# Kernel optimization log

Measured on AMD Instinct MI355X. Metric: run time of the kernel, lower is better.

Reference implementation:

```python
import jax, jax.numpy as jnp
import numpy as np

DIM = 512
HID = 2048
BLOCKS = 4
VOCAB = 32000
HEADS = 8
HD = DIM // HEADS
B = 4
T = 257
MBS = 64
LR = 3e-4
EPS = 1e-5


def setup_inputs() -> dict:
    key = jax.random.key(0)
    ks = jax.random.split(key, 10)
    s = 0.02
    n = lambda k, shp: jax.random.normal(k, shp, dtype=jnp.float32) * s
    return {
        'x': jax.random.randint(ks[0], (B, T), 0, VOCAB),
        'embed': n(ks[1], (VOCAB, DIM)),
        'pos': n(ks[2], (MBS, DIM)),
        'ln1_g': jnp.ones((BLOCKS, DIM), jnp.float32),
        'ln1_b': jnp.zeros((BLOCKS, DIM), jnp.float32),
        'qkv_w': n(ks[3], (BLOCKS, DIM, 3 * DIM)),
        'qkv_b': jnp.zeros((BLOCKS, 3 * DIM), jnp.float32),
        'proj_w': n(ks[4], (BLOCKS, DIM, DIM)),
        'proj_b': jnp.zeros((BLOCKS, DIM), jnp.float32),
        'ln2_g': jnp.ones((BLOCKS, DIM), jnp.float32),
        'ln2_b': jnp.zeros((BLOCKS, DIM), jnp.float32),
        'mlp_w1': n(ks[5], (BLOCKS, DIM, HID)),
        'mlp_b1': jnp.zeros((BLOCKS, HID), jnp.float32),
        'mlp_w2': n(ks[6], (BLOCKS, HID, DIM)),
        'mlp_b2': jnp.zeros((BLOCKS, DIM), jnp.float32),
        'lnf_g': jnp.ones((DIM,), jnp.float32),
        'lnf_b': jnp.zeros((DIM,), jnp.float32),
        'head_w': n(ks[7], (DIM, VOCAB)),
        'head_b': jnp.zeros((VOCAB,), jnp.float32),
    }


def _ln(x, g, b):
    m = x.mean(-1, keepdims=True)
    v = ((x - m) ** 2).mean(-1, keepdims=True)
    return (x - m) * jax.lax.rsqrt(v + EPS) * g + b


def _transformer(tokens, static, dyn):
    (embed, pos, ln1_g, ln1_b, qkv_w, qkv_b, proj_w, proj_b,
     ln2_g, ln2_b, lnf_g, lnf_b, head_w, head_b) = static
    mw1, mb1, mw2, mb2 = dyn
    Bx, L = tokens.shape
    h = embed[tokens] + pos[:L]                      # [B, L, D]
    mask = jnp.tril(jnp.ones((L, L), dtype=bool))
    for i in range(BLOCKS):
        xn = _ln(h, ln1_g[i], ln1_b[i])
        qkv = xn @ qkv_w[i] + qkv_b[i]               # [B, L, 3D]
        q, k, v = jnp.split(qkv, 3, axis=-1)
        hd = lambda t: t.reshape(Bx, L, HEADS, HD).transpose(0, 2, 1, 3)
        q, k, v = hd(q), hd(k), hd(v)                # [B, H, L, Dh]
        s = jnp.einsum('bhqd,bhkd->bhqk', q, k) / np.float32(np.sqrt(HD))
        s = jnp.where(mask, s, jnp.float32(-1e9))
        a = jax.nn.softmax(s, axis=-1)
        o = jnp.einsum('bhqk,bhkd->bhqd', a, v).transpose(0, 2, 1, 3).reshape(Bx, L, DIM)
        h = h + o @ proj_w[i] + proj_b[i]
        xn2 = _ln(h, ln2_g[i], ln2_b[i])
        h = h + jax.nn.gelu(xn2 @ mw1[i] + mb1[i]) @ mw2[i] + mb2[i]
    h = _ln(h, lnf_g, lnf_b)
    return h @ head_w + head_b                       # [B, L, V]


def reference(x, embed, pos, ln1_g, ln1_b, qkv_w, qkv_b, proj_w, proj_b,
              ln2_g, ln2_b, mlp_w1, mlp_b1, mlp_w2, mlp_b2,
              lnf_g, lnf_b, head_w, head_b):
    static = (embed, pos, ln1_g, ln1_b, qkv_w, qkv_b, proj_w, proj_b,
              ln2_g, ln2_b, lnf_g, lnf_b, head_w, head_b)
    dyn0 = (mlp_w1, mlp_b1, mlp_w2, mlp_b2)
    n_chunks = (T - 1) // MBS
    inp = x[:, :T - 1].reshape(B, n_chunks, MBS).transpose(1, 0, 2)  # [C, B, b]
    tgt = x[:, 1:T].reshape(B, n_chunks, MBS).transpose(1, 0, 2)

    def step(dyn, chunk):
        ci, ct = chunk
        def loss_fn(d):
            logits = _transformer(ci, static, d)
            logp = jax.nn.log_softmax(logits, axis=-1)
            nll = -jnp.take_along_axis(logp, ct[..., None], axis=-1).squeeze(-1).mean()
            return nll, logits
        grads, logits = jax.grad(loss_fn, has_aux=True)(dyn)
        new_dyn = jax.tree_util.tree_map(lambda p, g: p - LR * g, dyn, grads)
        return new_dyn, logits

    _, logit_chunks = jax.lax.scan(step, dyn0, (inp, tgt))   # [C, B, b, V]
    return logit_chunks.transpose(1, 0, 2, 3).reshape(B, (T - 1), VOCAB)
```

## Files before the change

### kernel.cpp

```cpp
#include <hip/hip_runtime.h>
#include <cstddef>

#define LRATE 3e-4f

typedef short short8 __attribute__((ext_vector_type(8)));
typedef float f32x4 __attribute__((ext_vector_type(4)));
typedef __bf16 bf16x8 __attribute__((ext_vector_type(8)));

__device__ __forceinline__ unsigned short f2b(float f){
  unsigned u = __builtin_bit_cast(unsigned, f);
  unsigned r = (u + 0x7fffu + ((u>>16)&1u)) >> 16;
  return (unsigned short)r;
}
__device__ __forceinline__ float b2f(unsigned short s){
  unsigned u = ((unsigned)s)<<16;
  return __builtin_bit_cast(float, u);
}
__device__ __forceinline__ float gelu_f(float x){
  float u = 0.7978845608028654f*(x + 0.044715f*x*x*x);
  float t = tanhf(u);
  return 0.5f*x*(1.f+t);
}
__device__ __forceinline__ float gelu_df(float x){
  float x2 = x*x;
// ... 89 lines not shown

  STAGE(0,0);
  for(int t=0;t<k_iters;++t){
    int buf=t&1;
    STAGE(t+1<k_iters?t+1:t, buf^1);
    asm volatile("" ::: "memory");
    constexpr int VMC = LNA ? (TILE/32) : (TILE/16);
    if constexpr(VMC==2)      asm volatile("s_waitcnt vmcnt(2)" ::: "memory");
    else if constexpr(VMC==4) asm volatile("s_waitcnt vmcnt(4)" ::: "memory");
    else                      asm volatile("s_waitcnt vmcnt(8)" ::: "memory");
    __builtin_amdgcn_sched_barrier(0);
    __builtin_amdgcn_s_barrier();
    asm volatile("" ::: "memory");
    const char* Ab=(const char*)(Asm+buf*TILE*64);
    const char* Bb=(const char*)(Bsm+buf*TILE*64);
    #pragma unroll
    for(int h=0;h<2;h++){
      bf16x8 af[F], bfr[F];
      #pragma unroll
      for(int fa=0;fa<F;fa++){
        int row=wr*(TILE/2)+fa*16+r16;
        int c=(h*4+kg)^(row&7);
        af[fa]=__builtin_bit_cast(bf16x8, *(const short8*)(Ab + row*128 + c*16));
      }
      #pragma unroll
      for(int fb=0;fb<F;fb++){
        int row=wc*(TILE/2)+fb*16+r16;
        int c=(h*4+kg)^(row&7);
        bfr[fb]=__builtin_bit_cast(bf16x8, *(const short8*)(Bb + row*128 + c*16));
      }
      #pragma unroll
      for(int fa=0;fa<F;fa++)
        #pragma unroll
        for(int fb=0;fb<F;fb++)
          acc[fa][fb]=__builtin_amdgcn_mfma_f32_16x16x32_bf16(af[fa],bfr[fb],acc[fa][fb],0,0,0);
    }
    asm volatile("s_waitcnt lgkmcnt(0)" ::: "memory");
    __builtin_amdgcn_sched_barrier(0);
    __builtin_amdgcn_s_barrier();
    asm volatile("" ::: "memory");
  }
  asm volatile("s_waitcnt vmcnt(0)" ::: "memory");

  int rb = lane>>4;
  float st1[F][4]={}, st2[F][4]={};
  #pragma unroll
  for(int fa=0; fa<F; fa++){
    #pragma unroll
    for(int fb=0; fb<F; fb++){
      f32x4 av = acc[fa][fb];
      #pragma unroll
      for(int i=0;i<4;i++){
        int m = bm + wr*(TILE/2) + fa*16 + rb*4 + i;
        int n = bn + wc*(TILE/2) + fb*16 + r16;
        float v = av[i];
        if(bias) v += bias[n];
        if(resid) v += resid[(size_t)m*N + n];
        if(zsrc) v *= gelu_df(zsrc[(size_t)m*N + n]);
        if constexpr(STATS){ st1[fa][i] += v; st2[fa][i] += v*v; }
        int mo = (remap_c>=0)? ((m>>6)*256 + remap_c*64 + (m&63)) : m;
        if(outf) outf[(size_t)blockIdx.z*M*N + (size_t)mo*N + n] = v;
        if(outb) outb[(size_t)mo*N + n] = f2b(gelu_b ? gelu_f(v) : v);
      }
    }
  }
  if constexpr(STATS){
    #pragma unroll
    for(int fa=0; fa<F; fa++){
      #pragma unroll
      for(int i=0;i<4;i++){
        float s1 = st1[fa][i], s2 = st2[fa][i];
        #pragma unroll
        for(int msk=1; msk<16; msk<<=1){ s1 += __shfl_xor(s1,msk); s2 += __shfl_xor(s2,msk); }
        if(r16==0){
          int m = bm + wr*(TILE/2) + fa*16 + rb*4 + i;
          atomicAdd(&oS1[m], s1);
          atomicAdd(&oS2[m], s2);
        }
      }
    }
  }
}

template<int LNA, int STATS>
__global__ __launch_bounds__(256) void k_nt32(
    const unsigned short* __restrict__ Ag,
    const float* __restrict__ Af, const float* __restrict__ aS1, const float* __restrict__ aS2,
    const float* __restrict__ lng, const float* __restrict__ lnb,
    const unsigned short* __restrict__ Bg,
    const float* __restrict__ bias, const float* __restrict__ resid, const float* __restrict__ zsrc,
    float* __restrict__ outf, unsigned short* __restrict__ outb,
    float* __restrict__ oS1, float* __restrict__ oS2,
    int M, int N, int K, int k_iters, int gelu_b)
{
  __shared__ __align__(16) short Asl[8*2048];
  __shared__ __align__(16) short Bsl[8*2048];
  int tid=threadIdx.x, lane=tid&63, w=tid>>6;
  int wr=w>>1, wc=w&1, r16=lane&15, kg=lane>>4;
  int bn=blockIdx.x*32, bm=blockIdx.y*32;
  int row=tid>>3, s8=tid&7, gc=s8^(row&7);
  f32x4 acc={0.f,0.f,0.f,0.f};

  auto ISSUE_A=[&](int t,int slot){
    gll16(Ag + (size_t)(bm+row)*K + t*64 + gc*8, (char*)Asl + slot*4096 + tid*16);
  };
  auto ISSUE_B=[&](int t,int slot){
    gll16(Bg + (size_t)(bn+row)*K + t*64 + gc*8, (char*)Bsl + slot*4096 + tid*16);
  };

  if constexpr(LNA){
    float mm, rr;
    { float a=aS1[bm+row], b=aS2[bm+row]; mm=a*(1.f/512.f); rr=rsqrtf(b*(1.f/512.f)-mm*mm+1e-5f); }
    for(int t=0;t<k_iters;t++){
      const float* src = Af + (size_t)(bm+row)*K + t*64 + gc*8;
      float4 v0=*(const float4*)src, v1=*(const float4*)(src+4);
      const float* gp=lng+t*64+gc*8; const float* bp=lnb+t*64+gc*8;
      float4 g0=*(const float4*)gp, g1=*(const float4*)(gp+4);
      float4 c0=*(const float4*)bp, c1=*(const float4*)(bp+4);
      short8 o;
      o[0]=(short)f2b((v0.x-mm)*rr*g0.x+c0.x);
      o[1]=(short)f2b((v0.y-mm)*rr*g0.y+c0.y);
      o[2]=(short)f2b((v0.z-mm)*rr*g0.z+c0.z);
      o[3]=(short)f2b((v0.w-mm)*rr*g0.w+c0.w);
      o[4]=(short)f2b((v1.x-mm)*rr*g1.x+c1.x);
      o[5]=(short)f2b((v1.y-mm)*rr*g1.y+c1.y);
      o[6]=(short)f2b((v1.z-mm)*rr*g1.z+c1.z);
      o[7]=(short)f2b((v1.w-mm)*rr*g1.w+c1.w);
      *(short8*)((char*)Asl + t*4096 + tid*16) = o;
    }
  }

  #pragma unroll
  for(int s=0;s<6;s++){
    if constexpr(LNA==0) ISSUE_A(s, s);
    ISSUE_B(s, s);
  }
  if constexpr(LNA){
    asm volatile("s_waitcnt lgkmcnt(0)" ::: "memory");
    __builtin_amdgcn_sched_barrier(0);
    __builtin_amdgcn_s_barrier();
  }

  for(int t=0;t<k_iters;++t){
    int tt = (t+6<k_iters)? t+6 : k_iters-1;
    int slot=(t+6)&7;
    if constexpr(LNA==0) ISSUE_A(tt, slot);
    ISSUE_B(tt, slot);
    if constexpr(LNA==0) asm volatile("s_waitcnt vmcnt(12)" ::: "memory");
    else                 asm volatile("s_waitcnt vmcnt(6)" ::: "memory");
    __builtin_amdgcn_sched_barrier(0);
    __builtin_amdgcn_s_barrier();
    __builtin_amdgcn_sched_barrier(0);
    const char* Ab = LNA ? (const char*)Asl + t*4096 : (const char*)Asl + (t&7)*4096;
    const char* Bb = (const char*)Bsl + (t&7)*4096;
    #pragma unroll
    for(int h=0;h<2;h++){
      int rowa=wr*16+r16, ca=(h*4+kg)^(rowa&7);
      bf16x8 a=__builtin_bit_cast(bf16x8, *(const short8*)(Ab + rowa*128 + ca*16));
      int rowb=wc*16+r16, cb=(h*4+kg)^(rowb&7);
      bf16x8 b=__builtin_bit_cast(bf16x8, *(const short8*)(Bb + rowb*128 + cb*16));
      acc=__builtin_amdgcn_mfma_f32_16x16x32_bf16(a,b,acc,0,0,0);
    }
    asm volatile("s_waitcnt lgkmcnt(0)" ::: "memory");
    __builtin_amdgcn_sched_barrier(0);
  }
  asm volatile("s_waitcnt vmcnt(0)" ::: "memory");

  int rb=lane>>4;
  float st1[4]={}, st2[4]={};
  #pragma unroll
  for(int i=0;i<4;i++){
    int m = bm + wr*16 + rb*4 + i;
    int n = bn + wc*16 + r16;
    float v = acc[i];
    if(bias) v += bias[n];
    if(resid) v += resid[(size_t)m*N + n];
    if(zsrc) v *= gelu_df(zsrc[(size_t)m*N + n]);
    if constexpr(STATS){ st1[i]=v; st2[i]=v*v; }
    if(outf) outf[(size_t)m*N + n] = v;
    if(outb) outb[(size_t)m*N + n] = f2b(gelu_b ? gelu_f(v) : v);
  }
  if constexpr(STATS){
    #pragma unroll
    for(int i=0;i<4;i++){
      float s1=st1[i], s2=st2[i];
      #pragma unroll
      for(int msk=1;msk<16;msk<<=1){ s1+=__shfl_xor(s1,msk); s2+=__shfl_xor(s2,msk); }
      if(r16==0){
        int m = bm + wr*16 + rb*4 + i;
        atomicAdd(&oS1[m], s1);
        atomicAdd(&oS2[m], s2);
      }
    }
  }
}

template<int LNA>
__device__ __forceinline__ void sgd_body(
    const unsigned short* __restrict__ Ag,
    const float* __restrict__ Af, const float* __restrict__ aS1, const float* __restrict__ aS2,
    const float* __restrict__ lng, const float* __restrict__ lnb,
    const unsigned short* __restrict__ Bg,
    float* __restrict__ Wf, unsigned short* __restrict__ Wb, unsigned short* __restrict__ Wt,
    float* __restrict__ bv, int M, int N, int bm, int bn,
    short* Asm, short* Bsm, short* Tsm)
{
  int tid = threadIdx.x;
  f32x4 acc00={},acc01={},acc10={},acc11={};
  int lane = tid&63, w = tid>>6, wr = w>>1, wc = w&1;
  int r16 = lane&15, kg = lane>>4;
  float gv[8], bvv[8];
  if constexpr(LNA){
    int ms=(tid&7)*8;
    #pragma unroll
    for(int j=0;j<8;j++){ gv[j]=lng[bm+ms+j]; bvv[j]=lnb[bm+ms+j]; }
  }
  float csum = 0.f;
  int docs = (bv && bm==0 && tid<64);
  for(int k0=0; k0<256; k0+=32){
    if constexpr(LNA==0){
      int kk = tid>>3, ms=(tid&7)*8;
      short8 v = *(const short8*)(Ag + (size_t)(k0+kk)*M + bm + ms);
      #pragma unroll
      for(int j=0;j<8;j++){ int row=ms+j; Asm[row*40 + (((kk>>3)^((row>>3)&3))<<3) + (kk&7)] = v[j]; }
    } else {
      int kk = tid>>3, ms=(tid&7)*8;
      int token = k0+kk;
      float s1=aS1[token], s2=aS2[token];
      float mm=s1*(1.f/512.f);
      float rr=rsqrtf(s2*(1.f/512.f)-mm*mm+1e-5f);
      const float* src = Af + (size_t)token*M + bm + ms;
      float4 v0=*(const float4*)src, v1=*(const float4*)(src+4);
      float vals[8]={v0.x,v0.y,v0.z,v0.w,v1.x,v1.y,v1.z,v1.w};
      #pragma unroll
      for(int j=0;j<8;j++){
        int row=ms+j;
// ... 253 lines not shown
    __builtin_amdgcn_sched_barrier(0);
  }
  asm volatile("s_waitcnt vmcnt(0)" ::: "memory");
  __syncthreads();

  #pragma unroll
  for(int fa=0;fa<2;fa++)
    #pragma unroll
    for(int fb=0;fb<3;fb++)
      #pragma unroll
      for(int i=0;i<4;i++){
        int row=wr*32+fa*16+rb*4+i;
        int band=wc*3+fb;
        int p=band>>2, cin=(band&3)*16+r16;
        float v = acc[fa][fb][i] + bias[p*512 + hh*64 + cin];
        unsigned short bv16 = f2b(v);
        qkB[(size_t)(bb*64+row)*1536 + p*512 + hh*64 + cin] = bv16;
        if(p==0)      tr_write(Qs,  row, cin, bv16);
        else if(p==1) tr_write(Ks2, row, cin, bv16);
        else          tr_write(Vt,  cin, row, bv16);
      }
  __syncthreads();

  int wr2=w>>2, wc2=w&3;
  f32x4 sa[2]={};
  #pragma unroll
  for(int h=0;h<2;h++){
    bf16x8 bfr = frag_read(Ks2, wc2*16+r16, h, kg);
    #pragma unroll
    for(int fa=0;fa<2;fa++){
      bf16x8 af = frag_read(Qs, wr2*32+fa*16+r16, h, kg);
      sa[fa]=__builtin_amdgcn_mfma_f32_16x16x32_bf16(af,bfr,sa[fa],0,0,0);
    }
  }
  #pragma unroll
  for(int fa=0;fa<2;fa++)
    #pragma unroll
    for(int i=0;i<4;i++){
      int row=wr2*32+fa*16+rb*4+i, col=wc2*16+r16;
      Sf[row*68+col] = (col<=row) ? sa[fa][i]*0.125f : -1e9f;
    }
  __syncthreads();

  {
    int srow=tid>>3, seg8=tid&7;
    float vals[8]; float mx=-3.4e38f;
    #pragma unroll
    for(int k2=0;k2<8;k2++){ vals[k2]=Sf[srow*68+seg8*8+k2]; mx=fmaxf(mx,vals[k2]); }
    mx=fmaxf(mx,__shfl_xor(mx,1)); mx=fmaxf(mx,__shfl_xor(mx,2)); mx=fmaxf(mx,__shfl_xor(mx,4));
    float sm=0;
    #pragma unroll
    for(int k2=0;k2<8;k2++){ vals[k2]=expf(vals[k2]-mx); sm+=vals[k2]; }
    sm+=__shfl_xor(sm,1); sm+=__shfl_xor(sm,2); sm+=__shfl_xor(sm,4);
    float inv=1.f/sm;
    short8 p0;
    #pragma unroll
    for(int k2=0;k2<8;k2++) p0[k2]=(short)f2b(vals[k2]*inv);
    __syncthreads();
    *(short8*)((char*)Pb + srow*128 + (((seg8)^(srow&7))<<4)) = p0;
    *(short8*)(ap + ((size_t)(bb*8+hh)*64 + srow)*64 + seg8*8) = p0;
  }
  __syncthreads();

  f32x4 oa[2]={};
  #pragma unroll
  for(int h=0;h<2;h++){
    bf16x8 bfr = frag_read(Vt, wc2*16+r16, h, kg);
    #pragma unroll
    for(int fa=0;fa<2;fa++){
      bf16x8 af = frag_read(Pb, wr2*32+fa*16+r16, h, kg);
      oa[fa]=__builtin_amdgcn_mfma_f32_16x16x32_bf16(af,bfr,oa[fa],0,0,0);
    }
  }
  #pragma unroll
  for(int fa=0;fa<2;fa++)
    #pragma unroll
    for(int i=0;i<4;i++){
      int row=wr2*32+fa*16+rb*4+i, col=wc2*16+r16;
      obuf[(size_t)(bb*64+row)*512 + hh*64 + col] = f2b(oa[fa][i]);
    }
}

__global__ __launch_bounds__(512) void k_do_attn(
    const unsigned short* __restrict__ dhBb, const unsigned short* __restrict__ projwB,
    const unsigned short* __restrict__ qkvB, const unsigned short* __restrict__ ap,
    unsigned short* __restrict__ dqkv)
{
  __shared__ __align__(16) short Asl[4*4096];
  __shared__ __align__(16) short Bsl2[4*4096];
  __shared__ __align__(16) short dOs[4096], Vs[4096], Kt[4096], Qt[4096], dOt[4096], Pt[4096], dsN[4096], dsT[4096];
  __shared__ float rsum[64][2];
  float* Pacc = (float*)Asl;
  int hh=blockIdx.x, bb=blockIdx.y;
  int tid=threadIdx.x, lane=tid&63, w=tid>>6;
  int wg=w>>2, wl=w&3;
  int wr=wl>>1, wc=wl&1, r16=lane&15, kg=lane>>4, rb=lane>>4;
  const unsigned short* qbase = qkvB + (size_t)bb*64*1536 + hh*64;
  const unsigned short* abase = ap + (size_t)(bb*8+hh)*64*64;

  {
    int row=tid>>3, gc=(tid&7)^(row&7);
    gll16(qbase + 1024 + (size_t)row*1536 + gc*8, (char*)Vs + tid*16);
  }
  {
    int row=tid>>3, c8=tid&7;
    short8 kreg=*(const short8*)(qbase+512+(size_t)row*1536+c8*8);
    short8 qreg=*(const short8*)(qbase+(size_t)row*1536+c8*8);
    short8 preg=*(const short8*)(abase+(size_t)row*64+c8*8);
    #pragma unroll
    for(int j=0;j<8;j++){
      int col=c8*8+j;
      tr_write(Kt, col, row, (unsigned short)kreg[j]);
      tr_write(Qt, col, row, (unsigned short)qreg[j]);
      tr_write(Pt, col, row, (unsigned short)preg[j]);
    }
  }

  const unsigned short* Bg = projwB + (size_t)(hh*64)*512;
  auto STAGE=[&](int t,int buf){
    int k0=(wg*4+t)*64;
    #pragma unroll
    for(int q=0;q<2;q++){
      int id=wl*128+q*64+lane, row=id>>3, gc=(id&7)^(row&7);
      gll16(dhBb + (size_t)(bb*64+row)*512 + k0 + gc*8, (char*)Asl + (wg*2+buf)*8192 + id*16);
      gll16(Bg + (size_t)row*512 + k0 + gc*8, (char*)Bsl2 + (wg*2+buf)*8192 + id*16);
    }
  };
  STAGE(0,0);
  f32x4 acc[2][2]={};
  for(int t=0;t<4;t++){
    int buf=t&1;
    STAGE(t+1<4?t+1:t, buf^1);
    asm volatile("s_waitcnt vmcnt(4)" ::: "memory");
    __builtin_amdgcn_sched_barrier(0);
    __builtin_amdgcn_s_barrier();
    __builtin_amdgcn_sched_barrier(0);
    const char* Ab=(const char*)Asl + (wg*2+buf)*8192;
    const char* Bb=(const char*)Bsl2 + (wg*2+buf)*8192;
    #pragma unroll
    for(int h=0;h<2;h++){
      bf16x8 af[2], bfr[2];
      #pragma unroll
      for(int f=0;f<2;f++){
        int rowa=wr*32+f*16+r16, ca=(h*4+kg)^(rowa&7);
        af[f]=__builtin_bit_cast(bf16x8, *(const short8*)(Ab + rowa*128 + ca*16));
        int rowb=wc*32+f*16+r16, cb=(h*4+kg)^(rowb&7);
        bfr[f]=__builtin_bit_cast(bf16x8, *(const short8*)(Bb + rowb*128 + cb*16));
      }
      #pragma unroll
      for(int fa=0;fa<2;fa++)
        #pragma unroll
        for(int fb=0;fb<2;fb++)
          acc[fa][fb]=__builtin_amdgcn_mfma_f32_16x16x32_bf16(af[fa],bfr[fb],acc[fa][fb],0,0,0);
    }
    asm volatile("s_waitcnt lgkmcnt(0)" ::: "memory");
    __builtin_amdgcn_sched_barrier(0);
    __builtin_amdgcn_s_barrier();
    __builtin_amdgcn_sched_barrier(0);
  }
  asm volatile("s_waitcnt vmcnt(0)" ::: "memory");
  __syncthreads();

  if(wg==1){
    #pragma unroll
    for(int fa=0;fa<2;fa++)
      #pragma unroll
      for(int fb=0;fb<2;fb++)
        #pragma unroll
        for(int i=0;i<4;i++){
          int row=wr*32+fa*16+rb*4+i, col=wc*32+fb*16+r16;
          Pacc[row*64+col]=acc[fa][fb][i];
        }
  }
  __syncthreads();
  if(wg==0){
    #pragma unroll
    for(int fa=0;fa<2;fa++)
      #pragma unroll
      for(int fb=0;fb<2;fb++)
        #pragma unroll
        for(int i=0;i<4;i++){
          int row=wr*32+fa*16+rb*4+i, col=wc*32+fb*16+r16;
          unsigned short db = f2b(acc[fa][fb][i] + Pacc[row*64+col]);
          tr_write(dOs, row, col, db);
          tr_write(dOt, col, row, db);
        }
  }
  __syncthreads();

  f32x4 da[2][2]={};
  float pv[2][2][4];
  if(wg==0){
    #pragma unroll
    for(int h=0;h<2;h++){
      bf16x8 af[2], bfr[2];
      #pragma unroll
      for(int f=0;f<2;f++){ af[f]=frag_read(dOs, wr*32+f*16+r16, h, kg); bfr[f]=frag_read(Vs, wc*32+f*16+r16, h, kg); }
      #pragma unroll
      for(int fa=0;fa<2;fa++)
        #pragma unroll
        for(int fb=0;fb<2;fb++)
          da[fa][fb]=__builtin_amdgcn_mfma_f32_16x16x32_bf16(af[fa],bfr[fb],da[fa][fb],0,0,0);
    }
    float part[2][4]={};
    #pragma unroll
    for(int fa=0;fa<2;fa++)
      #pragma unroll
      for(int i=0;i<4;i++){
        #pragma unroll
        for(int fb=0;fb<2;fb++){
          int row=wr*32+fa*16+rb*4+i, col=wc*32+fb*16+r16;
          float p = b2f(*(const unsigned short*)((const char*)Pt + col*128 + (((row>>3)^(col&7))<<4) + (row&7)*2));
          pv[fa][fb][i]=p;
          part[fa][i] += p*da[fa][fb][i];
        }
        float s=part[fa][i];
        #pragma unroll
        for(int msk=1;msk<16;msk<<=1) s += __shfl_xor(s,msk);
        if(r16==0) rsum[wr*32+fa*16+rb*4+i][wc]=s;
      }
  } else {
    f32x4 dvv[2][2]={};
    #pragma unroll
    for(int h=0;h<2;h++){
      bf16x8 af[2], bfr[2];
      #pragma unroll
      for(int f=0;f<2;f++){ af[f]=frag_read(Pt, wr*32+f*16+r16, h, kg); bfr[f]=frag_read(dOt, wc*32+f*16+r16, h, kg); }
      #pragma unroll
      for(int fa=0;fa<2;fa++)
        #pragma unroll
        for(int fb=0;fb<2;fb++)
          dvv[fa][fb]=__builtin_amdgcn_mfma_f32_16x16x32_bf16(af[fa],bfr[fb],dvv[fa][fb],0,0,0);
    }
    #pragma unroll
    for(int fa=0;fa<2;fa++)
      #pragma unroll
      for(int fb=0;fb<2;fb++)
        #pragma unroll
        for(int i=0;i<4;i++){
          int row=wr*32+fa*16+rb*4+i, col=wc*32+fb*16+r16;
          dqkv[(size_t)(bb*64+row)*1536 + hh*64 + 1024 + col] = f2b(dvv[fa][fb][i]);
        }
  }
  __syncthreads();

  if(wg==0){
    #pragma unroll
    for(int fa=0;fa<2;fa++)
      #pragma unroll
      for(int fb=0;fb<2;fb++)
        #pragma unroll
        for(int i=0;i<4;i++){
          int row=wr*32+fa*16+rb*4+i, col=wc*32+fb*16+r16;
          float rt = rsum[row][0]+rsum[row][1];
          float ds = pv[fa][fb][i]*(da[fa][fb][i]-rt)*0.125f;
// ... 49 lines not shown
  #pragma unroll
  for(int off=32;off;off>>=1) mx = fmaxf(mx, __shfl_xor(mx,off));
  if(lane==0) red[w]=mx;
  __syncthreads();
  float m = red[0];
  #pragma unroll
  for(int i=1;i<16;i++) m = fmaxf(m, red[i]);
  __syncthreads();

  float s=0;
  for(int v=tid; v<32000; v+=1024){ float e = expf(b2f(eb[v])-m); s+=e; eb[v]=f2b(e); }
  #pragma unroll
  for(int off=32;off;off>>=1) s += __shfl_xor(s,off);
  if(lane==0) red[w]=s;
  __syncthreads();
  float tot = 0.f;
  #pragma unroll
  for(int i=0;i<16;i++) tot += red[i];
  float iz = 1.f/tot * (1.f/256.f);

  unsigned short* dr = dlog + (size_t)n*32000;
  for(int v=tid; v<32000; v+=1024){
    float a = b2f(eb[v])*iz;
    if(v==tgt) a -= (1.f/256.f);
    dr[v] = f2b(a);
  }
}

extern "C" void kernel_launch(void* const* d_in, const int* in_sizes, int n_in,
                              void* d_out, int out_size, void* d_ws, size_t ws_size,
                              hipStream_t stream)
{
  const int*   x      = (const int*)d_in[0];
  const float* embed  = (const float*)d_in[1];
  const float* pos    = (const float*)d_in[2];
  const float* ln1_g  = (const float*)d_in[3];
  const float* ln1_b  = (const float*)d_in[4];
  const float* qkv_w  = (const float*)d_in[5];
  const float* qkv_b  = (const float*)d_in[6];
  const float* proj_w = (const float*)d_in[7];
  const float* proj_b = (const float*)d_in[8];
  const float* ln2_g  = (const float*)d_in[9];
  const float* ln2_b  = (const float*)d_in[10];
  const float* mlp_w1 = (const float*)d_in[11];
  const float* mlp_b1 = (const float*)d_in[12];
  const float* mlp_w2 = (const float*)d_in[13];
  const float* mlp_b2 = (const float*)d_in[14];
  const float* lnf_g  = (const float*)d_in[15];
  const float* lnf_b  = (const float*)d_in[16];
  const float* head_w = (const float*)d_in[17];
  const float* head_b = (const float*)d_in[18];
  float* out = (float*)d_out;

  char* base = (char*)d_ws;
  size_t off = 0;
  auto AB = [&](size_t bytes)->char*{ char* p = base + off; off += (bytes + 255) & ~(size_t)255; return p; };
  float* W1c  = (float*)AB(16777216);
  float* W2c  = (float*)AB(16777216);
  float* B1c  = (float*)AB(32768);
  float* B2c  = (float*)AB(8192);
  float* hin  = (float*)AB(5*524288);
  float* h1s  = (float*)AB(4*524288);
  float* z1s  = (float*)AB(4*2097152);
  float* dhA  = (float*)AB(524288);
  float* dhB  = (float*)AB(524288);
  float* dxn  = (float*)AB(524288);
  float* dpart= (float*)AB(50*524288);
  float* stats= (float*)AB(4*9*2*256*4);
  unsigned short* qkvwB = (unsigned short*)AB(6291456);
  unsigned short* qkvwT = (unsigned short*)AB(6291456);
  unsigned short* projwB= (unsigned short*)AB(2097152);
  unsigned short* projwT= (unsigned short*)AB(2097152);
  unsigned short* headwB= (unsigned short*)AB(32768000);
  unsigned short* headwT= (unsigned short*)AB(32768000);
  unsigned short* W1b   = (unsigned short*)AB(8388608);
  unsigned short* W1t   = (unsigned short*)AB(8388608);
  unsigned short* W2b   = (unsigned short*)AB(8388608);
  unsigned short* W2t   = (unsigned short*)AB(8388608);
  unsigned short* z1gs  = (unsigned short*)AB(4194304);
  unsigned short* qkBs  = (unsigned short*)AB(4*786432);
  unsigned short* apBs  = (unsigned short*)AB(4*262144);
  unsigned short* obufB = (unsigned short*)AB(262144);
  unsigned short* dlogB = (unsigned short*)AB(16384000);
  unsigned short* dhbB  = (unsigned short*)AB(5*262144);
  unsigned short* dhBb  = (unsigned short*)AB(262144);
  unsigned short* dz1bs = (unsigned short*)AB(4*1048576);
  unsigned short* dqkvB = (unsigned short*)AB(786432);

  auto SS1 = [&](int c, int s)->float*{ return stats + ((size_t)(c*9+s)*2)*256; };
  auto SS2 = [&](int c, int s)->float*{ return stats + ((size_t)(c*9+s)*2)*256 + 256; };

  k_setup<<<72,256,0,stream>>>(stats, B1c, mlp_b1, B2c, mlp_b2);
  k_cvt_t<<<dim3(24,8,4),256,0,stream>>>(qkv_w, qkvwT, qkvwB, nullptr, 512, 1536);
  k_cvt_t<<<dim3(8,8,4),256,0,stream>>>(proj_w, projwT, projwB, nullptr, 512, 512);
  k_cvt_t<<<dim3(500,8,1),256,0,stream>>>(head_w, headwT, headwB, nullptr, 512, 32000);
  k_cvt_t<<<dim3(32,8,4),256,0,stream>>>(mlp_w1, W1t, W1b, W1c, 512, 2048);
  k_cvt_t<<<dim3(8,32,4),256,0,stream>>>(mlp_w2, W2t, W2b, W2c, 2048, 512);

  for(int c=0;c<4;c++){
    k_embed<<<256,256,0,stream>>>(x, embed, pos, hin, SS1(c,0), SS2(c,0), c);
    for(int i=0;i<4;i++){
      float* h0 = hin + (size_t)i*131072;
      float* h2 = hin + (size_t)(i+1)*131072;
      float* h1 = h1s + (size_t)i*131072;
      float* z1 = z1s + (size_t)i*524288;
      unsigned short* z1g = z1gs + (size_t)i*524288;
      unsigned short* qkB = qkBs + (size_t)i*393216;
      unsigned short* apB = apBs + (size_t)i*131072;
      k_qkv_attn<<<dim3(8,4),512,0,stream>>>(h0, SS1(c,i), SS2(c,i), ln1_g+i*512, ln1_b+i*512,
          qkvwT+(size_t)i*786432, qkv_b+i*1536, qkB, obufB, apB);
      k_nt32<0,1><<<dim3(16,8),256,0,stream>>>(obufB, nullptr, nullptr, nullptr, nullptr, nullptr,
          projwT+(size_t)i*262144, proj_b+i*512, h0, nullptr,
          h1, nullptr, SS1(c,5+i), SS2(c,5+i), 256,512,512, 8, 0);
      k_nt32<1,0><<<dim3(64,8),256,0,stream>>>(nullptr, h1, SS1(c,5+i), SS2(c,5+i), ln2_g+i*512, ln2_b+i*512,
          W1t+(size_t)i*1048576, B1c+i*2048, nullptr, nullptr,
          z1, z1g, nullptr, nullptr, 256,2048,512, 8, 1);
      k_nt32<0,1><<<dim3(16,8),256,0,stream>>>(z1g, nullptr, nullptr, nullptr, nullptr, nullptr,
          W2t+(size_t)i*1048576, B2c+i*512, h1, nullptr,
          h2, nullptr, SS1(c,i+1), SS2(c,i+1), 256,512,2048, 32, 0);
    }
    k_nt<128,1,0><<<dim3(250,2),256,0,stream>>>(nullptr, hin+4*131072, SS1(c,4), SS2(c,4), lnf_g, lnf_b,
        headwT, head_b, nullptr, nullptr,
        out, nullptr, nullptr, nullptr, 256,32000,512, 8, 0, c);

    k_ce_dlog<<<256,1024,0,stream>>>(out, x, dlogB, c);
    k_nt<128,0,0><<<dim3(4,2,50),256,0,stream>>>(dlogB, nullptr, nullptr, nullptr, nullptr, nullptr,
        headwB, nullptr, nullptr, nullptr,
        dpart, nullptr, nullptr, nullptr, 256,512,32000, 10, 0, -1);
    k_ln_bwd<<<256,256,0,stream>>>(nullptr, dpart, 50, hin+4*131072, lnf_g, SS1(c,4), SS2(c,4),
        nullptr, dhA, dhbB + 3*131072);
    for(int i=3;i>=0;i--){
      float* h0 = hin + (size_t)i*131072;
      float* h1 = h1s + (size_t)i*131072;
      float* z1 = z1s + (size_t)i*524288;
      unsigned short* qkB = qkBs + (size_t)i*393216;
      unsigned short* apB = apBs + (size_t)i*131072;
      k_nt32<0,0><<<dim3(64,8),256,0,stream>>>(dhbB + (size_t)i*131072, nullptr, nullptr, nullptr, nullptr, nullptr,
          W2b+(size_t)i*1048576, nullptr, nullptr, z1,
          nullptr, dz1bs + (size_t)i*524288, nullptr, nullptr, 256,2048,512, 8, 0);
      k_nt32<0,0><<<dim3(16,8),256,0,stream>>>(dz1bs + (size_t)i*524288, nullptr, nullptr, nullptr, nullptr, nullptr,
          W1b+(size_t)i*1048576, nullptr, nullptr, nullptr,
          dxn, nullptr, nullptr, nullptr, 256,512,2048, 32, 0);
      k_ln_bwd<<<256,256,0,stream>>>(dxn, nullptr, 0, h1, ln2_g+i*512, SS1(c,5+i), SS2(c,5+i),
          dhA, dhB, dhBb);
      k_do_attn<<<dim3(8,4),512,0,stream>>>(dhBb, projwB+(size_t)i*262144, qkB, apB, dqkvB);
      k_nt32<0,0><<<dim3(16,8),256,0,stream>>>(dqkvB, nullptr, nullptr, nullptr, nullptr, nullptr,
          qkvwB+(size_t)i*786432, nullptr, nullptr, nullptr,
          dxn, nullptr, nullptr, nullptr, 256,512,1536, 24, 0);
      k_ln_bwd<<<256,256,0,stream>>>(dxn, nullptr, 0, h0, ln1_g+i*512, SS1(c,i), SS2(c,i),
          dhB, dhA, dhbB + (size_t)((i==0)?4:i-1)*131072);
    }
    k_sgd_all<<<2048,256,0,stream>>>(z1gs, dhbB, dz1bs, h1s, stats, c,
        W1c, W1b, W1t, B1c, W2c, W2b, W2t, B2c, ln2_g, ln2_b);
  }
}
```

Baseline: 2.364 ms.

## Fuse LayerNorm backward into the following backward GEMM and attention kernels

Removes the standalone k_ln_bwd launches in the backward pass. LN2 backward is computed inside k_do_attn's prologue, which builds the bf16 A operand in shared memory. LN1 backward of the next-higher layer moves into a new LNB variant of k_nt32 that builds its bf16 A tile in LDS. One block per row tile also writes the fp32 and bf16 residual gradients to global memory. This trades fewer launches and intermediate round trips for redundant LN-backward recomputation in every column block, plus higher LDS use in k_do_attn.

```diff
diff --git a/kernel.cpp b/kernel.cpp
--- a/kernel.cpp
+++ b/kernel.cpp
@@ -195,7 +195,7 @@
   }
 }
 
-template<int LNA, int STATS>
+template<int LNA, int STATS, int LNB>
 __global__ __launch_bounds__(256) void k_nt32(
     const unsigned short* __restrict__ Ag,
     const float* __restrict__ Af, const float* __restrict__ aS1, const float* __restrict__ aS2,
@@ -204,6 +204,8 @@
     const float* __restrict__ bias, const float* __restrict__ resid, const float* __restrict__ zsrc,
     float* __restrict__ outf, unsigned short* __restrict__ outb,
     float* __restrict__ oS1, float* __restrict__ oS2,
+    const float* __restrict__ dyf, const float* __restrict__ adn,
+    float* __restrict__ oA, unsigned short* __restrict__ oB2,
     int M, int N, int K, int k_iters, int gelu_b)
 {
   __shared__ __align__(16) short Asl[8*2048];
@@ -220,6 +222,62 @@
   auto ISSUE_B=[&](int t,int slot){
     gll16(Bg + (size_t)(bn+row)*K + t*64 + gc*8, (char*)Bsl + slot*4096 + tid*16);
   };
+
+  if constexpr(LNB){
+    #pragma unroll
+    for(int s=0;s<6;s++) ISSUE_B(s, s);
+    int grow = bm + row;
+    float s1v=aS1[grow], s2v=aS2[grow];
+    float m=s1v*(1.f/512.f);
+    float r=rsqrtf(s2v*(1.f/512.f)-m*m+1e-5f);
+    float sgh=0.f, sghx=0.f;
+    for(int t=0;t<k_iters;t++){
+      const float* dyp=dyf+(size_t)grow*512+t*64+gc*8;
+      const float* xp =Af +(size_t)grow*512+t*64+gc*8;
+      const float* gp =lng+t*64+gc*8;
+      float4 a0=*(const float4*)dyp, a1=*(const float4*)(dyp+4);
+      float4 x0=*(const float4*)xp,  x1=*(const float4*)(xp+4);
+      float4 g0=*(const float4*)gp,  g1=*(const float4*)(gp+4);
+      float dys[8]={a0.x,a0.y,a0.z,a0.w,a1.x,a1.y,a1.z,a1.w};
+      float xs[8]={x0.x,x0.y,x0.z,x0.w,x1.x,x1.y,x1.z,x1.w};
+      float gs[8]={g0.x,g0.y,g0.z,g0.w,g1.x,g1.y,g1.z,g1.w};
+      #pragma unroll
+      for(int j=0;j<8;j++){ float gh=dys[j]*gs[j]; float xh=(xs[j]-m)*r; sgh+=gh; sghx+=gh*xh; }
+    }
+    sgh +=__shfl_xor(sgh,1);  sgh +=__shfl_xor(sgh,2);  sgh +=__shfl_xor(sgh,4);
+    sghx+=__shfl_xor(sghx,1); sghx+=__shfl_xor(sghx,2); sghx+=__shfl_xor(sghx,4);
+    float mg=sgh*(1.f/512.f), mgx=sghx*(1.f/512.f);
+    for(int t=0;t<k_iters;t++){
+      const float* dyp=dyf+(size_t)grow*512+t*64+gc*8;
+      const float* xp =Af +(size_t)grow*512+t*64+gc*8;
+      const float* gp =lng+t*64+gc*8;
+      const float* ap2=adn+(size_t)grow*512+t*64+gc*8;
+      float4 a0=*(const float4*)dyp, a1=*(const float4*)(dyp+4);
+      float4 x0=*(const float4*)xp,  x1=*(const float4*)(xp+4);
+      float4 g0=*(const float4*)gp,  g1=*(const float4*)(gp+4);
+      float4 d0=*(const float4*)ap2, d1=*(const float4*)(ap2+4);
+      float dys[8]={a0.x,a0.y,a0.z,a0.w,a1.x,a1.y,a1.z,a1.w};
+      float xs[8]={x0.x,x0.y,x0.z,x0.w,x1.x,x1.y,x1.z,x1.w};
+      float gs[8]={g0.x,g0.y,g0.z,g0.w,g1.x,g1.y,g1.z,g1.w};
+      float ads[8]={d0.x,d0.y,d0.z,d0.w,d1.x,d1.y,d1.z,d1.w};
+      float dv[8];
+      short8 o;
+      #pragma unroll
+      for(int j=0;j<8;j++){
+        float gh=dys[j]*gs[j]; float xh=(xs[j]-m)*r;
+        dv[j]=(gh-mg-xh*mgx)*r + ads[j];
+        o[j]=(short)f2b(dv[j]);
+      }
+      *(short8*)((char*)Asl + t*4096 + tid*16) = o;
+      if(blockIdx.x==0){
+        float4 w0={dv[0],dv[1],dv[2],dv[3]}, w1={dv[4],dv[5],dv[6],dv[7]};
+        *(float4*)(oA+(size_t)grow*512+t*64+gc*8) = w0;
+        *(float4*)(oA+(size_t)grow*512+t*64+gc*8+4) = w1;
+        *(short8*)(oB2+(size_t)grow*512+t*64+gc*8) = o;
+      }
+    }
+    __syncthreads();
+  }
 
   if constexpr(LNA){
     float mm, rr;
@@ -243,10 +301,12 @@
     }
   }
 
-  #pragma unroll
-  for(int s=0;s<6;s++){
-    if constexpr(LNA==0) ISSUE_A(s, s);
-    ISSUE_B(s, s);
+  if constexpr(!LNB){
+    #pragma unroll
+    for(int s=0;s<6;s++){
+      if constexpr(LNA==0) ISSUE_A(s, s);
+      ISSUE_B(s, s);
+    }
   }
   if constexpr(LNA){
     asm volatile("s_waitcnt lgkmcnt(0)" ::: "memory");
@@ -254,17 +314,18 @@
     __builtin_amdgcn_s_barrier();
   }
 
+  constexpr int ARES = (LNA||LNB);
   for(int t=0;t<k_iters;++t){
     int tt = (t+6<k_iters)? t+6 : k_iters-1;
     int slot=(t+6)&7;
-    if constexpr(LNA==0) ISSUE_A(tt, slot);
+    if constexpr(!ARES) ISSUE_A(tt, slot);
     ISSUE_B(tt, slot);
-    if constexpr(LNA==0) asm volatile("s_waitcnt vmcnt(12)" ::: "memory");
-    else                 asm volatile("s_waitcnt vmcnt(6)" ::: "memory");
+    if constexpr(!ARES) asm volatile("s_waitcnt vmcnt(12)" ::: "memory");
+    else                asm volatile("s_waitcnt vmcnt(6)" ::: "memory");
     __builtin_amdgcn_sched_barrier(0);
     __builtin_amdgcn_s_barrier();
     __builtin_amdgcn_sched_barrier(0);
-    const char* Ab = LNA ? (const char*)Asl + t*4096 : (const char*)Asl + (t&7)*4096;
+    const char* Ab = ARES ? (const char*)Asl + t*4096 : (const char*)Asl + (t&7)*4096;
     const char* Bb = (const char*)Bsl + (t&7)*4096;
     #pragma unroll
     for(int h=0;h<2;h++){
@@ -684,15 +745,25 @@
 }
 
 __global__ __launch_bounds__(512) void k_do_attn(
-    const unsigned short* __restrict__ dhBb, const unsigned short* __restrict__ projwB,
+    const float* __restrict__ dxn, const float* __restrict__ h1,
+    const float* __restrict__ g2, const float* __restrict__ S1, const float* __restrict__ S2,
+    const float* __restrict__ addin, float* __restrict__ dhB,
+    const unsigned short* __restrict__ projwB,
     const unsigned short* __restrict__ qkvB, const unsigned short* __restrict__ ap,
     unsigned short* __restrict__ dqkv)
 {
-  __shared__ __align__(16) short Asl[4*4096];
+  __shared__ __align__(16) short Afull[32768];
   __shared__ __align__(16) short Bsl2[4*4096];
-  __shared__ __align__(16) short dOs[4096], Vs[4096], Kt[4096], Qt[4096], dOt[4096], Pt[4096], dsN[4096], dsT[4096];
+  __shared__ __align__(16) short Vs[4096];
   __shared__ float rsum[64][2];
-  float* Pacc = (float*)Asl;
+  short* dOs = Afull;
+  short* Kt  = Afull + 4096;
+  short* Qt  = Afull + 8192;
+  short* dOt = Afull + 12288;
+  short* Pt  = Afull + 16384;
+  short* dsN = Afull + 20480;
+  short* dsT = Afull + 24576;
+  float* Pacc = (float*)Bsl2;
   int hh=blockIdx.x, bb=blockIdx.y;
   int tid=threadIdx.x, lane=tid&63, w=tid>>6;
   int wg=w>>2, wl=w&3;
@@ -700,44 +771,86 @@
   const unsigned short* qbase = qkvB + (size_t)bb*64*1536 + hh*64;
   const unsigned short* abase = ap + (size_t)(bb*8+hh)*64*64;
 
+  int row8=tid>>3, c8=tid&7, gc8=c8^(row8&7);
+  gll16(qbase + 1024 + (size_t)row8*1536 + gc8*8, (char*)Vs + tid*16);
+  short8 kreg=*(const short8*)(qbase+512+(size_t)row8*1536+c8*8);
+  short8 qreg=*(const short8*)(qbase+(size_t)row8*1536+c8*8);
+  short8 preg=*(const short8*)(abase+(size_t)row8*64+c8*8);
+
+  const unsigned short* Bg = projwB + (size_t)(hh*64)*512;
+  auto STB=[&](int t,int buf){
+    #pragma unroll
+    for(int q=0;q<2;q++){
+      int id=wl*128+q*64+lane, brow=id>>3, bgc=(id&7)^(brow&7);
+      gll16(Bg + (size_t)brow*512 + (wg*4+t)*64 + bgc*8, (char*)Bsl2 + (wg*2+buf)*8192 + id*16);
+    }
+  };
+  STB(0,0);
+
   {
-    int row=tid>>3, gc=(tid&7)^(row&7);
-    gll16(qbase + 1024 + (size_t)row*1536 + gc*8, (char*)Vs + tid*16);
-  }
-  {
-    int row=tid>>3, c8=tid&7;
-    short8 kreg=*(const short8*)(qbase+512+(size_t)row*1536+c8*8);
-    short8 qreg=*(const short8*)(qbase+(size_t)row*1536+c8*8);
-    short8 preg=*(const short8*)(abase+(size_t)row*64+c8*8);
-    #pragma unroll
-    for(int j=0;j<8;j++){
-      int col=c8*8+j;
-      tr_write(Kt, col, row, (unsigned short)kreg[j]);
-      tr_write(Qt, col, row, (unsigned short)qreg[j]);
-      tr_write(Pt, col, row, (unsigned short)preg[j]);
-    }
-  }
-
-  const unsigned short* Bg = projwB + (size_t)(hh*64)*512;
-  auto STAGE=[&](int t,int buf){
-    int k0=(wg*4+t)*64;
-    #pragma unroll
-    for(int q=0;q<2;q++){
-      int id=wl*128+q*64+lane, row=id>>3, gc=(id&7)^(row&7);
-      gll16(dhBb + (size_t)(bb*64+row)*512 + k0 + gc*8, (char*)Asl + (wg*2+buf)*8192 + id*16);
-      gll16(Bg + (size_t)row*512 + k0 + gc*8, (char*)Bsl2 + (wg*2+buf)*8192 + id*16);
-    }
-  };
-  STAGE(0,0);
+    int grow = bb*64 + row8;
+    float s1v=S1[grow], s2v=S2[grow];
+    float m=s1v*(1.f/512.f);
+    float r=rsqrtf(s2v*(1.f/512.f)-m*m+1e-5f);
+    float sgh=0.f, sghx=0.f;
+    #pragma unroll
+    for(int t=0;t<8;t++){
+      const float* dyp = dxn + (size_t)grow*512 + t*64 + gc8*8;
+      const float* xp  = h1  + (size_t)grow*512 + t*64 + gc8*8;
+      const float* gp  = g2  + t*64 + gc8*8;
+      float4 a0=*(const float4*)dyp, a1=*(const float4*)(dyp+4);
+      float4 x0=*(const float4*)xp,  x1=*(const float4*)(xp+4);
+      float4 g0=*(const float4*)gp,  g1=*(const float4*)(gp+4);
+      float dys[8]={a0.x,a0.y,a0.z,a0.w,a1.x,a1.y,a1.z,a1.w};
+      float xs[8]={x0.x,x0.y,x0.z,x0.w,x1.x,x1.y,x1.z,x1.w};
+      float gs[8]={g0.x,g0.y,g0.z,g0.w,g1.x,g1.y,g1.z,g1.w};
+      #pragma unroll
+      for(int j=0;j<8;j++){ float gh=dys[j]*gs[j]; float xh=(xs[j]-m)*r; sgh+=gh; sghx+=gh*xh; }
+    }
+    sgh +=__shfl_xor(sgh,1);  sgh +=__shfl_xor(sgh,2);  sgh +=__shfl_xor(sgh,4);
+    sghx+=__shfl_xor(sghx,1); sghx+=__shfl_xor(sghx,2); sghx+=__shfl_xor(sghx,4);
+    float mg=sgh*(1.f/512.f), mgx=sghx*(1.f/512.f);
+    #pragma unroll
+    for(int t=0;t<8;t++){
+      const float* dyp = dxn + (size_t)grow*512 + t*64 + gc8*8;
+      const float* xp  = h1  + (size_t)grow*512 + t*64 + gc8*8;
+      const float* gp  = g2  + t*64 + gc8*8;
+      const float* ap2 = addin + (size_t)grow*512 + t*64 + gc8*8;
+      float4 a0=*(const float4*)dyp, a1=*(const float4*)(dyp+4);
+      float4 x0=*(const float4*)xp,  x1=*(const float4*)(xp+4);
+      float4 g0=*(const float4*)gp,  g1=*(const float4*)(gp+4);
+      float4 d0=*(const float4*)ap2, d1=*(const float4*)(ap2+4);
+      float dys[8]={a0.x,a0.y,a0.z,a0.w,a1.x,a1.y,a1.z,a1.w};
+      float xs[8]={x0.x,x0.y,x0.z,x0.w,x1.x,x1.y,x1.z,x1.w};
+      float gs[8]={g0.x,g0.y,g0.z,g0.w,g1.x,g1.y,g1.z,g1.w};
+      float ads[8]={d0.x,d0.y,d0.z,d0.w,d1.x,d1.y,d1.z,d1.w};
+      float dv[8];
+      short8 o;
+      #pragma unroll
+      for(int j=0;j<8;j++){
+        float gh=dys[j]*gs[j]; float xh=(xs[j]-m)*r;
+        dv[j]=(gh-mg-xh*mgx)*r + ads[j];
+        o[j]=(short)f2b(dv[j]);
+      }
+      *(short8*)((char*)Afull + t*8192 + tid*16) = o;
+      if(hh==0){
+        float4 w0={dv[0],dv[1],dv[2],dv[3]}, w1={dv[4],dv[5],dv[6],dv[7]};
+        *(float4*)(dhB + (size_t)grow*512 + t*64 + gc8*8) = w0;
+        *(float4*)(dhB + (size_t)grow*512 + t*64 + gc8*8 + 4) = w1;
+      }
+    }
+  }
+  __syncthreads();
+
   f32x4 acc[2][2]={};
   for(int t=0;t<4;t++){
     int buf=t&1;
-    STAGE(t+1<4?t+1:t, buf^1);
-    asm volatile("s_waitcnt vmcnt(4)" ::: "memory");
+    STB(t+1<4?t+1:t, buf^1);
+    asm volatile("s_waitcnt vmcnt(2)" ::: "memory");
     __builtin_amdgcn_sched_barrier(0);
     __builtin_amdgcn_s_barrier();
     __builtin_amdgcn_sched_barrier(0);
-    const char* Ab=(const char*)Asl + (wg*2+buf)*8192;
+    const char* Ab=(const char*)Afull + (wg*4+t)*8192;
     const char* Bb=(const char*)Bsl2 + (wg*2+buf)*8192;
     #pragma unroll
     for(int h=0;h<2;h++){
@@ -773,6 +886,13 @@
           int row=wr*32+fa*16+rb*4+i, col=wc*32+fb*16+r16;
           Pacc[row*64+col]=acc[fa][fb][i];
         }
+  }
+  #pragma unroll
+  for(int j=0;j<8;j++){
+    int col=c8*8+j;
+    tr_write(Kt, col, row8, (unsigned short)kreg[j]);
+    tr_write(Qt, col, row8, (unsigned short)qreg[j]);
+    tr_write(Pt, col, row8, (unsigned short)preg[j]);
   }
   __syncthreads();
   if(wg==0){
@@ -988,8 +1108,7 @@
   unsigned short* apBs  = (unsigned short*)AB(4*262144);
   unsigned short* obufB = (unsigned short*)AB(262144);
   unsigned short* dlogB = (unsigned short*)AB(16384000);
-  unsigned short* dhbB  = (unsigned short*)AB(5*262144);
-  unsigned short* dhBb  = (unsigned short*)AB(262144);
+  unsigned short* dhbB  = (unsigned short*)AB(4*262144);
   unsigned short* dz1bs = (unsigned short*)AB(4*1048576);
   unsigned short* dqkvB = (unsigned short*)AB(786432);
 
@@ -1015,15 +1134,18 @@
       unsigned short* apB = apBs + (size_t)i*131072;
       k_qkv_attn<<<dim3(8,4),512,0,stream>>>(h0, SS1(c,i), SS2(c,i), ln1_g+i*512, ln1_b+i*512,
           qkvwT+(size_t)i*786432, qkv_b+i*1536, qkB, obufB, apB);
-      k_nt32<0,1><<<dim3(16,8),256,0,stream>>>(obufB, nullptr, nullptr, nullptr, nullptr, nullptr,
+      k_nt32<0,1,0><<<dim3(16,8),256,0,stream>>>(obufB, nullptr, nullptr, nullptr, nullptr, nullptr,
           projwT+(size_t)i*262144, proj_b+i*512, h0, nullptr,
-          h1, nullptr, SS1(c,5+i), SS2(c,5+i), 256,512,512, 8, 0);
-      k_nt32<1,0><<<dim3(64,8),256,0,stream>>>(nullptr, h1, SS1(c,5+i), SS2(c,5+i), ln2_g+i*512, ln2_b+i*512,
+          h1, nullptr, SS1(c,5+i), SS2(c,5+i),
+          nullptr, nullptr, nullptr, nullptr, 256,512,512, 8, 0);
+      k_nt32<1,0,0><<<dim3(64,8),256,0,stream>>>(nullptr, h1, SS1(c,5+i), SS2(c,5+i), ln2_g+i*512, ln2_b+i*512,
           W1t+(size_t)i*1048576, B1c+i*2048, nullptr, nullptr,
-          z1, z1g, nullptr, nullptr, 256,2048,512, 8, 1);
-      k_nt32<0,1><<<dim3(16,8),256,0,stream>>>(z1g, nullptr, nullptr, nullptr, nullptr, nullptr,
+          z1, z1g, nullptr, nullptr,
+          nullptr, nullptr, nullptr, nullptr, 256,2048,512, 8, 1);
+      k_nt32<0,1,0><<<dim3(16,8),256,0,stream>>>(z1g, nullptr, nullptr, nullptr, nullptr, nullptr,
           W2t+(size_t)i*1048576, B2c+i*512, h1, nullptr,
-          h2, nullptr, SS1(c,i+1), SS2(c,i+1), 256,512,2048, 32, 0);
+          h2, nullptr, SS1(c,i+1), SS2(c,i+1),
+          nullptr, nullptr, nullptr, nullptr, 256,512,2048, 32, 0);
     }
     k_nt<128,1,0><<<dim3(250,2),256,0,stream>>>(nullptr, hin+4*131072, SS1(c,4), SS2(c,4), lnf_g, lnf_b,
         headwT, head_b, nullptr, nullptr,
@@ -1041,20 +1163,28 @@
       float* z1 = z1s + (size_t)i*524288;
       unsigned short* qkB = qkBs + (size_t)i*393216;
       unsigned short* apB = apBs + (size_t)i*131072;
-      k_nt32<0,0><<<dim3(64,8),256,0,stream>>>(dhbB + (size_t)i*131072, nullptr, nullptr, nullptr, nullptr, nullptr,
-          W2b+(size_t)i*1048576, nullptr, nullptr, z1,
-          nullptr, dz1bs + (size_t)i*524288, nullptr, nullptr, 256,2048,512, 8, 0);
-      k_nt32<0,0><<<dim3(16,8),256,0,stream>>>(dz1bs + (size_t)i*524288, nullptr, nullptr, nullptr, nullptr, nullptr,
+      if(i==3){
+        k_nt32<0,0,0><<<dim3(64,8),256,0,stream>>>(dhbB + 3*131072, nullptr, nullptr, nullptr, nullptr, nullptr,
+            W2b+(size_t)i*1048576, nullptr, nullptr, z1,
+            nullptr, dz1bs + (size_t)i*524288, nullptr, nullptr,
+            nullptr, nullptr, nullptr, nullptr, 256,2048,512, 8, 0);
+      } else {
+        k_nt32<0,0,1><<<dim3(64,8),256,0,stream>>>(nullptr, hin + (size_t)(i+1)*131072,
+            SS1(c,i+1), SS2(c,i+1), ln1_g+(i+1)*512, nullptr,
+            W2b+(size_t)i*1048576, nullptr, nullptr, z1,
+            nullptr, dz1bs + (size_t)i*524288, nullptr, nullptr,
+            dxn, dhB, dhA, dhbB + (size_t)i*131072, 256,2048,512, 8, 0);
+      }
+      k_nt32<0,0,0><<<dim3(16,8),256,0,stream>>>(dz1bs + (size_t)i*524288, nullptr, nullptr, nullptr, nullptr, nullptr,
           W1b+(size_t)i*1048576, nullptr, nullptr, nullptr,
-          dxn, nullptr, nullptr, nullptr, 256,512,2048, 32, 0);
-      k_ln_bwd<<<256,256,0,stream>>>(dxn, nullptr, 0, h1, ln2_g+i*512, SS1(c,5+i), SS2(c,5+i),
-          dhA, dhB, dhBb);
-      k_do_attn<<<dim3(8,4),512,0,stream>>>(dhBb, projwB+(size_t)i*262144, qkB, apB, dqkvB);
-      k_nt32<0,0><<<dim3(16,8),256,0,stream>>>(dqkvB, nullptr, nullptr, nullptr, nullptr, nullptr,
+          dxn, nullptr, nullptr, nullptr,
+          nullptr, nullptr, nullptr, nullptr, 256,512,2048, 32, 0);
+      k_do_attn<<<dim3(8,4),512,0,stream>>>(dxn, h1, ln2_g+i*512, SS1(c,5+i), SS2(c,5+i),
+          dhA, dhB, projwB+(size_t)i*262144, qkB, apB, dqkvB);
+      k_nt32<0,0,0><<<dim3(16,8),256,0,stream>>>(dqkvB, nullptr, nullptr, nullptr, nullptr, nullptr,
           qkvwB+(size_t)i*786432, nullptr, nullptr, nullptr,
-          dxn, nullptr, nullptr, nullptr, 256,512,1536, 24, 0);
-      k_ln_bwd<<<256,256,0,stream>>>(dxn, nullptr, 0, h0, ln1_g+i*512, SS1(c,i), SS2(c,i),
-          dhB, dhA, dhbB + (size_t)((i==0)?4:i-1)*131072);
+          dxn, nullptr, nullptr, nullptr,
+          nullptr, nullptr, nullptr, nullptr, 256,512,1536, 24, 0);
     }
     k_sgd_all<<<2048,256,0,stream>>>(z1gs, dhbB, dz1bs, h1s, stats, c,
         W1c, W1b, W1t, B1c, W2c, W2b, W2t, B2c, ln2_g, ln2_b);
```

After: 2.582 ms. 9.2% more time.
